# Optimization experiments

Measured on AMD Instinct MI355X. Metric: run time of the kernel, lower is better.

## Reference

```python
import jax, jax.numpy as jnp
import numpy as np

B, D, E, T, P = 65536, 256, 256, 128, 8  # batch, memory_dim, edge_feat_dim, time_dim, num_prototypes
LN_EPS = 1e-6
NORM_EPS = 1e-6


def _layer_norm(x, w, b):
    mu = jnp.mean(x, axis=-1, keepdims=True)
    var = jnp.mean(jnp.square(x - mu), axis=-1, keepdims=True)
    return (x - mu) / jnp.sqrt(var + LN_EPS) * w + b


def setup_inputs() -> dict:
    key = jax.random.key(0)
    ks = jax.random.split(key, 10)
    qin = D + E + T            # query_proj in_features
    gin = 2 * D + T            # gate_proj in_features
    return {
        "raw_memory": jax.random.normal(ks[0], (B, D), dtype=jnp.float32),
        "node_features": jax.random.normal(ks[1], (B, D), dtype=jnp.float32),
        "edge_features": jax.random.normal(ks[2], (B, E), dtype=jnp.float32),
        "time_encoding": jax.random.normal(ks[3], (B, T), dtype=jnp.float32),
        "prototypes": jax.random.normal(ks[4], (B, P, D), dtype=jnp.float32),
        # learned params (xavier gain=0.1 -> small)
        "Wq": jax.random.normal(ks[5], (D, qin), dtype=jnp.float32) * (0.1 * np.sqrt(2.0 / (D + qin))),
        "bq": jnp.zeros((D,), dtype=jnp.float32),
        "Wg": jax.random.normal(ks[6], (1, gin), dtype=jnp.float32) * (0.1 * np.sqrt(2.0 / (1 + gin))),
        "bg": jnp.zeros((1,), dtype=jnp.float32),
        "temperature": jnp.ones((1,), dtype=jnp.float32),
        "ln_w": jnp.ones((D,), dtype=jnp.float32),
        "ln_b": jnp.zeros((D,), dtype=jnp.float32),
    }


def reference(raw_memory, node_features, edge_features, time_encoding, prototypes,
              Wq, bq, Wg, bg, temperature, ln_w, ln_b):
    # query projection (inputs are finite so _sanitize_tensor is identity)
    q_in = jnp.concatenate([raw_memory, edge_features, time_encoding], axis=-1)  # [B, D+E+T]
    query = jnp.tanh(_layer_norm(q_in @ Wq.T + bq, ln_w, ln_b))                   # [B, D]

    # cosine similarity to per-node prototypes (F.normalize uses max(norm, eps))
    qn = query / jnp.maximum(jnp.linalg.norm(query, axis=-1, keepdims=True), NORM_EPS)
    pn = prototypes / jnp.maximum(jnp.linalg.norm(prototypes, axis=-1, keepdims=True), NORM_EPS)
    sim = jnp.clip(jnp.einsum('bd,bpd->bp', qn, pn), -10.0, 10.0)                 # [B, P]
    temp = jnp.clip(temperature, 0.5, 5.0)
    sim = sim / (temp + 0.01)

    attn = jnp.clip(jax.nn.softmax(sim, axis=-1), 0.0, 1.0)                       # [B, P]
    candidate = jnp.clip(jnp.einsum('bp,bpd->bd', attn, prototypes), -5.0, 5.0)   # [B, D]

    # gated update
    g_in = jnp.clip(jnp.concatenate([raw_memory, candidate, time_encoding], axis=-1), -50.0, 50.0)
    gate = jax.nn.sigmoid(jnp.clip(g_in @ Wg.T + bg, -10.0, 10.0))                # [B, 1]
    updated = (1.0 - gate) * raw_memory + gate * candidate
    updated = jnp.clip(_layer_norm(updated, ln_w, ln_b), -10.0, 10.0)
    return updated
```

## Files before the change

### kernel.cpp

```cpp
#include <hip/hip_runtime.h>
#include <cstdint>
#include <cstddef>

#define D 256
#define E 256
#define T 128
#define QIN 640
#define P 8
#define R 16
#define KP 648
#define DP 260

typedef __attribute__((ext_vector_type(8))) short bf16x8;
typedef __attribute__((ext_vector_type(4))) float f32x4;

__device__ __forceinline__ ushort f2bf(float f) {
  uint32_t u = __float_as_uint(f);
  u += 0x7fffu + ((u >> 16) & 1u);
  return (ushort)(u >> 16);
}

__device__ __forceinline__ float rcpf(float x) { return __builtin_amdgcn_rcpf(x); }
__device__ __forceinline__ float rsqf(float x) { return __builtin_amdgcn_rsqf(x); }

__device__ __forceinline__ float fast_tanh(float x) {
  const float e = __expf(2.0f * x);
  return 1.0f - 2.0f * rcpf(e + 1.0f);
}

__device__ __forceinline__ float rsum32(float v) {
#pragma unroll
  for (int o = 16; o > 0; o >>= 1) v += __shfl_xor(v, o, 64);
  return v;
}
__device__ __forceinline__ void rsum32_2(float& a, float& b) {
#pragma unroll
  for (int o = 16; o > 0; o >>= 1) {
    a += __shfl_xor(a, o, 64);
    b += __shfl_xor(b, o, 64);
  }
}

__device__ __forceinline__ float clampf(float x, float lo, float hi) {
  return fminf(fmaxf(x, lo), hi);
}

__global__ void prep_w2_kernel(const float* __restrict__ Wq, ushort* __restrict__ W2) {
  const int idx = blockIdx.x * 256 + threadIdx.x;
  const int n = idx / QIN;
  const int k = idx - n * QIN;
  W2[((((k >> 3) * D + n) << 3)) + (k & 7)] = f2bf(Wq[idx]);
}

__device__ __forceinline__ bf16x8 cvt8(const float* p) {
  const float4 a = *(const float4*)p;
  const float4 b = *(const float4*)(p + 4);
  bf16x8 r;
  r[0] = (short)f2bf(a.x); r[1] = (short)f2bf(a.y);
  r[2] = (short)f2bf(a.z); r[3] = (short)f2bf(a.w);
  r[4] = (short)f2bf(b.x); r[5] = (short)f2bf(b.y);
  r[6] = (short)f2bf(b.z); r[7] = (short)f2bf(b.w);
  return r;
}

template <bool PRE>
__global__ __launch_bounds__(256, 4) void fused_kernel(
    const float* __restrict__ raw, const float* __restrict__ edge,
    const float* __restrict__ tim, const float* __restrict__ proto,
    const float* __restrict__ Wq, const ushort* __restrict__ W2,
    const float* __restrict__ bq, const float* __restrict__ Wg,
    const float* __restrict__ bg, const float* __restrict__ temp,
    const float* __restrict__ lnw, const float* __restrict__ lnb,
    float* __restrict__ out) {
  __shared__ ushort qa[R][KP];
  __shared__ float qpre[R][DP];

  const int tid = threadIdx.x;
  const int r0 = blockIdx.x * R;

#pragma unroll
  for (int it = 0; it < (R * QIN / 4) / 256; ++it) {
    const int flat = it * 256 + tid;
    const int r = flat / (QIN / 4);
    const int p4 = (flat - r * (QIN / 4)) * 4;
    const size_t g = (size_t)(r0 + r);
    float4 v;
    if (p4 < D)          v = *(const float4*)(raw + g * D + p4);
    else if (p4 < D + E) v = *(const float4*)(edge + g * E + (p4 - D));
    else                 v = *(const float4*)(tim + g * T + (p4 - D - E));
    ushort4 hh;
    hh.x = f2bf(v.x); hh.y = f2bf(v.y); hh.z = f2bf(v.z); hh.w = f2bf(v.w);
    *(ushort4*)&qa[r][p4] = hh;
  }
  __syncthreads();

  const int w = tid >> 6;
  const int lane = tid & 63;
  const int lr = lane & 15;
  const int lh = lane >> 4;

  {
    f32x4 acc[4];
#pragma unroll
    for (int c = 0; c < 4; ++c) acc[c] = (f32x4){0.f, 0.f, 0.f, 0.f};

    for (int kb = 0; kb < QIN; kb += 32) {
      const bf16x8 af = *(const bf16x8*)&qa[lr][kb + lh * 8];
#pragma unroll
      for (int c = 0; c < 4; ++c) {
        const int n = w * 64 + c * 16 + lr;
        bf16x8 bv;
        if (PRE) {
          bv = *(const bf16x8*)&W2[(((kb >> 3) + lh) * D + n) << 3];
        } else {
          bv = cvt8(Wq + (size_t)n * QIN + kb + lh * 8);
        }
        acc[c] = __builtin_amdgcn_mfma_f32_16x16x32_bf16(af, bv, acc[c], 0, 0, 0);
      }
    }
#pragma unroll
    for (int c = 0; c < 4; ++c) {
      const int n = w * 64 + c * 16 + lr;
      const float bqv = bq[n];
#pragma unroll
      for (int i = 0; i < 4; ++i) qpre[lh * 4 + i][n] = acc[c][i] + bqv;
    }
  }
  __syncthreads();

  const int h = lane >> 5;
  const int l32 = lane & 31;
  const int d0 = l32 * 4;
  const int d1 = d0 + 128;

  const float4 lw0 = *(const float4*)(lnw + d0);
  const float4 lw1 = *(const float4*)(lnw + d1);
  const float4 lb0 = *(const float4*)(lnb + d0);
  const float4 lb1 = *(const float4*)(lnb + d1);
  const float lwv[8] = {lw0.x, lw0.y, lw0.z, lw0.w, lw1.x, lw1.y, lw1.z, lw1.w};
  const float lbv[8] = {lb0.x, lb0.y, lb0.z, lb0.w, lb1.x, lb1.y, lb1.z, lb1.w};
  const float bgv = bg[0];
  const float invt = rcpf(clampf(temp[0], 0.5f, 5.0f) + 0.01f);

#pragma unroll
  for (int j = 0; j < 2; ++j) {
    const int r = j * 8 + w * 2 + h;
    const size_t g = (size_t)(r0 + r);
    const float* pb = proto + g * (size_t)(P * D);

    const float4 ra0 = *(const float4*)(raw + g * D + d0);
    const float4 ra1 = *(const float4*)(raw + g * D + d1);
    const float4 t4  = *(const float4*)(tim + g * T + d0);

    const float4 x0 = *(const float4*)&qpre[r][d0];
    const float4 x1 = *(const float4*)&qpre[r][d1];
    float x[8] = {x0.x, x0.y, x0.z, x0.w, x1.x, x1.y, x1.z, x1.w};
    float s = 0.f, ss = 0.f;
#pragma unroll
    for (int i = 0; i < 8; ++i) { s += x[i]; ss += x[i] * x[i]; }
    rsum32_2(s, ss);
    const float mu = s * (1.0f / 256.0f);
    const float var = ss * (1.0f / 256.0f) - mu * mu;
    const float rstd = rsqf(var + 1e-6f);
    float q[8];
    float qs = 0.f;
#pragma unroll
    for (int i = 0; i < 8; ++i) {
      q[i] = fast_tanh((x[i] - mu) * rstd * lwv[i] + lbv[i]);
      qs += q[i] * q[i];
    }

    float cv[8] = {0.f, 0.f, 0.f, 0.f, 0.f, 0.f, 0.f, 0.f};
    float us = 0.f;
    float rq = 0.f;
#pragma unroll
    for (int ch = 0; ch < 2; ++ch) {
      float4 A0[4], A1[4];
#pragma unroll
      for (int p = 0; p < 4; ++p) {
        A0[p] = *(const float4*)(pb + (size_t)(ch * 4 + p) * D + d0);
        A1[p] = *(const float4*)(pb + (size_t)(ch * 4 + p) * D + d1);
      }
      float dt[4], pn[4];
#pragma unroll
      for (int p = 0; p < 4; ++p) {
        dt[p] = q[0] * A0[p].x + q[1] * A0[p].y + q[2] * A0[p].z + q[3] * A0[p].w +
                q[4] * A1[p].x + q[5] * A1[p].y + q[6] * A1[p].z + q[7] * A1[p].w;
        pn[p] = A0[p].x * A0[p].x + A0[p].y * A0[p].y + A0[p].z * A0[p].z +
                A0[p].w * A0[p].w + A1[p].x * A1[p].x + A1[p].y * A1[p].y +
                A1[p].z * A1[p].z + A1[p].w * A1[p].w;
      }
#pragma unroll
      for (int o = 16; o > 0; o >>= 1) {
#pragma unroll
        for (int p = 0; p < 4; ++p) {
          dt[p] += __shfl_xor(dt[p], o, 64);
          pn[p] += __shfl_xor(pn[p], o, 64);
        }
        if (ch == 0) qs += __shfl_xor(qs, o, 64);
      }
      if (ch == 0) rq = fminf(rsqf(qs), 1e6f);

#pragma unroll
      for (int p = 0; p < 4; ++p) {
        const float rp = fminf(rsqf(pn[p]), 1e6f);
        const float sm = clampf(dt[p] * rq * rp, -10.0f, 10.0f) * invt;
        const float u = __expf(sm);
        us += u;
        cv[0] = fmaf(u, A0[p].x, cv[0]); cv[1] = fmaf(u, A0[p].y, cv[1]);
        cv[2] = fmaf(u, A0[p].z, cv[2]); cv[3] = fmaf(u, A0[p].w, cv[3]);
        cv[4] = fmaf(u, A1[p].x, cv[4]); cv[5] = fmaf(u, A1[p].y, cv[5]);
        cv[6] = fmaf(u, A1[p].z, cv[6]); cv[7] = fmaf(u, A1[p].w, cv[7]);
      }
    }
    const float sinv = rcpf(us);
    float cd[8];
#pragma unroll
    for (int i = 0; i < 8; ++i) cd[i] = clampf(cv[i] * sinv, -5.0f, 5.0f);

    const float rr[8] = {ra0.x, ra0.y, ra0.z, ra0.w, ra1.x, ra1.y, ra1.z, ra1.w};
    const float4 wr0 = *(const float4*)(Wg + d0);
    const float4 wr1 = *(const float4*)(Wg + d1);
    const float4 wc0 = *(const float4*)(Wg + D + d0);
    const float4 wc1 = *(const float4*)(Wg + D + d1);
    const float4 wt4 = *(const float4*)(Wg + 2 * D + d0);
    const float wrv[8] = {wr0.x, wr0.y, wr0.z, wr0.w, wr1.x, wr1.y, wr1.z, wr1.w};
    const float wcv[8] = {wc0.x, wc0.y, wc0.z, wc0.w, wc1.x, wc1.y, wc1.z, wc1.w};
    float gsum = clampf(t4.x, -50.f, 50.f) * wt4.x + clampf(t4.y, -50.f, 50.f) * wt4.y +
                 clampf(t4.z, -50.f, 50.f) * wt4.z + clampf(t4.w, -50.f, 50.f) * wt4.w;
#pragma unroll
    for (int i = 0; i < 8; ++i) {
      gsum += clampf(rr[i], -50.f, 50.f) * wrv[i];
      gsum += clampf(cd[i], -50.f, 50.f) * wcv[i];
    }
    const float z = clampf(rsum32(gsum) + bgv, -10.0f, 10.0f);
    const float gate = rcpf(1.0f + __expf(-z));

    float upd[8];
    float s2 = 0.f, ss2 = 0.f;
#pragma unroll
    for (int i = 0; i < 8; ++i) {
      upd[i] = (1.0f - gate) * rr[i] + gate * cd[i];
      s2 += upd[i]; ss2 += upd[i] * upd[i];
    }
    rsum32_2(s2, ss2);
    const float mu2 = s2 * (1.0f / 256.0f);
    const float var2 = ss2 * (1.0f / 256.0f) - mu2 * mu2;
    const float rstd2 = rsqf(var2 + 1e-6f);
    float4 y0, y1;
    y0.x = clampf((upd[0] - mu2) * rstd2 * lwv[0] + lbv[0], -10.0f, 10.0f);
    y0.y = clampf((upd[1] - mu2) * rstd2 * lwv[1] + lbv[1], -10.0f, 10.0f);
    y0.z = clampf((upd[2] - mu2) * rstd2 * lwv[2] + lbv[2], -10.0f, 10.0f);
    y0.w = clampf((upd[3] - mu2) * rstd2 * lwv[3] + lbv[3], -10.0f, 10.0f);
    y1.x = clampf((upd[4] - mu2) * rstd2 * lwv[4] + lbv[4], -10.0f, 10.0f);
    y1.y = clampf((upd[5] - mu2) * rstd2 * lwv[5] + lbv[5], -10.0f, 10.0f);
    y1.z = clampf((upd[6] - mu2) * rstd2 * lwv[6] + lbv[6], -10.0f, 10.0f);
    y1.w = clampf((upd[7] - mu2) * rstd2 * lwv[7] + lbv[7], -10.0f, 10.0f);
    *(float4*)(out + g * D + d0) = y0;
    *(float4*)(out + g * D + d1) = y1;
  }
}

extern "C" void kernel_launch(void* const* d_in, const int* in_sizes, int n_in,
                              void* d_out, int out_size, void* d_ws, size_t ws_size,
                              hipStream_t stream) {
  const float* raw   = (const float*)d_in[0];
  const float* edge  = (const float*)d_in[2];
  const float* tim   = (const float*)d_in[3];
  const float* proto = (const float*)d_in[4];
  const float* Wq    = (const float*)d_in[5];
  const float* bq    = (const float*)d_in[6];
  const float* Wg    = (const float*)d_in[7];
  const float* bg    = (const float*)d_in[8];
  const float* temp  = (const float*)d_in[9];
  const float* lnw   = (const float*)d_in[10];
  const float* lnb   = (const float*)d_in[11];
  float* out = (float*)d_out;

  const int B = in_sizes[0] / D;
  const int nblk = B / R;

  if (ws_size >= (size_t)QIN * D * sizeof(ushort)) {
    ushort* W2 = (ushort*)d_ws;
    prep_w2_kernel<<<(QIN * D) / 256, 256, 0, stream>>>(Wq, W2);
    fused_kernel<true><<<nblk, 256, 0, stream>>>(raw, edge, tim, proto, Wq, W2,
                                                 bq, Wg, bg, temp, lnw, lnb, out);
  } else {
    fused_kernel<false><<<nblk, 256, 0, stream>>>(raw, edge, tim, proto, Wq,
                                                  (const ushort*)nullptr, bq, Wg,
                                                  bg, temp, lnw, lnb, out);
  }
}
```

Before: 207.2 us.

## Software-pipeline row tiles: overlap next tile's MFMA GEMM with current epilogue

```diff
diff --git a/kernel.cpp b/kernel.cpp
--- a/kernel.cpp
+++ b/kernel.cpp
@@ -8,6 +8,7 @@
 #define QIN 640
 #define P 8
 #define R 16
+#define TILES 4
 #define KP 648
 #define DP 260
 
@@ -76,35 +77,44 @@
   __shared__ float qpre[R][DP];
 
   const int tid = threadIdx.x;
-  const int r0 = blockIdx.x * R;
-
-#pragma unroll
-  for (int it = 0; it < (R * QIN / 4) / 256; ++it) {
-    const int flat = it * 256 + tid;
-    const int r = flat / (QIN / 4);
-    const int p4 = (flat - r * (QIN / 4)) * 4;
-    const size_t g = (size_t)(r0 + r);
-    float4 v;
-    if (p4 < D)          v = *(const float4*)(raw + g * D + p4);
-    else if (p4 < D + E) v = *(const float4*)(edge + g * E + (p4 - D));
-    else                 v = *(const float4*)(tim + g * T + (p4 - D - E));
-    ushort4 hh;
-    hh.x = f2bf(v.x); hh.y = f2bf(v.y); hh.z = f2bf(v.z); hh.w = f2bf(v.w);
-    *(ushort4*)&qa[r][p4] = hh;
-  }
-  __syncthreads();
-
+  const int r0base = blockIdx.x * (TILES * R);
   const int w = tid >> 6;
   const int lane = tid & 63;
   const int lr = lane & 15;
   const int lh = lane >> 4;
-
-  {
-    f32x4 acc[4];
-#pragma unroll
-    for (int c = 0; c < 4; ++c) acc[c] = (f32x4){0.f, 0.f, 0.f, 0.f};
-
-    for (int kb = 0; kb < QIN; kb += 32) {
+  const int h = lane >> 5;
+  const int l32 = lane & 31;
+  const int d0 = l32 * 4;
+  const int d1 = d0 + 128;
+
+  const float4 lw0 = *(const float4*)(lnw + d0);
+  const float4 lw1 = *(const float4*)(lnw + d1);
+  const float4 lb0 = *(const float4*)(lnb + d0);
+  const float4 lb1 = *(const float4*)(lnb + d1);
+  const float lwv[8] = {lw0.x, lw0.y, lw0.z, lw0.w, lw1.x, lw1.y, lw1.z, lw1.w};
+  const float lbv[8] = {lb0.x, lb0.y, lb0.z, lb0.w, lb1.x, lb1.y, lb1.z, lb1.w};
+  const float bgv = bg[0];
+  const float invt = rcpf(clampf(temp[0], 0.5f, 5.0f) + 0.01f);
+
+  auto stage = [&](int r0) {
+#pragma unroll
+    for (int it = 0; it < (R * QIN / 4) / 256; ++it) {
+      const int flat = it * 256 + tid;
+      const int r = flat / (QIN / 4);
+      const int p4 = (flat - r * (QIN / 4)) * 4;
+      const size_t g = (size_t)(r0 + r);
+      float4 v;
+      if (p4 < D)          v = *(const float4*)(raw + g * D + p4);
+      else if (p4 < D + E) v = *(const float4*)(edge + g * E + (p4 - D));
+      else                 v = *(const float4*)(tim + g * T + (p4 - D - E));
+      ushort4 hh;
+      hh.x = f2bf(v.x); hh.y = f2bf(v.y); hh.z = f2bf(v.z); hh.w = f2bf(v.w);
+      *(ushort4*)&qa[r][p4] = hh;
+    }
+  };
+
+  auto kpart = [&](f32x4* acc, int kbeg, int kend) {
+    for (int kb = kbeg; kb < kend; kb += 32) {
       const bf16x8 af = *(const bf16x8*)&qa[lr][kb + lh * 8];
 #pragma unroll
       for (int c = 0; c < 4; ++c) {
@@ -118,6 +128,9 @@
         acc[c] = __builtin_amdgcn_mfma_f32_16x16x32_bf16(af, bv, acc[c], 0, 0, 0);
       }
     }
+  };
+
+  auto cstore = [&](f32x4* acc) {
 #pragma unroll
     for (int c = 0; c < 4; ++c) {
       const int n = w * 64 + c * 16 + lr;
@@ -125,25 +138,9 @@
 #pragma unroll
       for (int i = 0; i < 4; ++i) qpre[lh * 4 + i][n] = acc[c][i] + bqv;
     }
-  }
-  __syncthreads();
-
-  const int h = lane >> 5;
-  const int l32 = lane & 31;
-  const int d0 = l32 * 4;
-  const int d1 = d0 + 128;
-
-  const float4 lw0 = *(const float4*)(lnw + d0);
-  const float4 lw1 = *(const float4*)(lnw + d1);
-  const float4 lb0 = *(const float4*)(lnb + d0);
-  const float4 lb1 = *(const float4*)(lnb + d1);
-  const float lwv[8] = {lw0.x, lw0.y, lw0.z, lw0.w, lw1.x, lw1.y, lw1.z, lw1.w};
-  const float lbv[8] = {lb0.x, lb0.y, lb0.z, lb0.w, lb1.x, lb1.y, lb1.z, lb1.w};
-  const float bgv = bg[0];
-  const float invt = rcpf(clampf(temp[0], 0.5f, 5.0f) + 0.01f);
-
-#pragma unroll
-  for (int j = 0; j < 2; ++j) {
+  };
+
+  auto epi = [&](int r0, int j) {
     const int r = j * 8 + w * 2 + h;
     const size_t g = (size_t)(r0 + r);
     const float* pb = proto + g * (size_t)(P * D);
@@ -200,7 +197,6 @@
         if (ch == 0) qs += __shfl_xor(qs, o, 64);
       }
       if (ch == 0) rq = fminf(rsqf(qs), 1e6f);
-
 #pragma unroll
       for (int p = 0; p < 4; ++p) {
         const float rp = fminf(rsqf(pn[p]), 1e6f);
@@ -258,6 +254,40 @@
     y1.w = clampf((upd[7] - mu2) * rstd2 * lwv[7] + lbv[7], -10.0f, 10.0f);
     *(float4*)(out + g * D + d0) = y0;
     *(float4*)(out + g * D + d1) = y1;
+  };
+
+  stage(r0base);
+  __syncthreads();
+  {
+    f32x4 acc[4];
+#pragma unroll
+    for (int c = 0; c < 4; ++c) acc[c] = (f32x4){0.f, 0.f, 0.f, 0.f};
+    kpart(acc, 0, QIN);
+    __syncthreads();
+    cstore(acc);
+    stage(r0base + R);
+    __syncthreads();
+  }
+
+#pragma unroll 1
+  for (int t = 0; t < TILES; ++t) {
+    const int r0 = r0base + t * R;
+    if (t + 1 < TILES) {
+      f32x4 acc[4];
+#pragma unroll
+      for (int c = 0; c < 4; ++c) acc[c] = (f32x4){0.f, 0.f, 0.f, 0.f};
+      kpart(acc, 0, QIN / 2);
+      epi(r0, 0);
+      kpart(acc, QIN / 2, QIN);
+      epi(r0, 1);
+      __syncthreads();
+      cstore(acc);
+      if (t + 2 < TILES) stage(r0base + (t + 2) * R);
+      __syncthreads();
+    } else {
+      epi(r0, 0);
+      epi(r0, 1);
+    }
   }
 }
 
@@ -278,7 +308,7 @@
   float* out = (float*)d_out;
 
   const int B = in_sizes[0] / D;
-  const int nblk = B / R;
+  const int nblk = B / (R * TILES);
 
   if (ws_size >= (size_t)QIN * D * sizeof(ushort)) {
     ushort* W2 = (ushort*)d_ws;
```

New measurement: 606.5 us. 2.93x slower.
